# Kernel tuning notes

Measured on AMD Instinct MI355X. Metric: run time of the kernel, lower is better.

The kernel has to match this reference:

```python
import jax, jax.numpy as jnp
import numpy as np
from jax import lax

B, S, H, E, P, K, R = 64, 512, 768, 32, 16, 9, 6
HEADS, C1, C2 = 4, 128, 64
FEAT = 4 * C2 + 1  # e1, e2, e1*e2, context (64 each) + log-distance


def _ln(x, g, b):
    m = x.mean(-1, keepdims=True)
    v = ((x - m) ** 2).mean(-1, keepdims=True)
    return (x - m) * lax.rsqrt(v + 1e-5) * g + b


def _gat(x, adj, W, a_s, a_d, bias, heads, cout, concat):
    # Dense GATConv over a small fully-masked entity graph. adj[b,i,j]=edge j->i (incl. self-loops).
    h = jnp.einsum('bef,fhc->behc', x, W.reshape(x.shape[-1], heads, cout))
    s = jnp.einsum('behc,hc->bhe', h, a_s)  # source-node attention term
    d = jnp.einsum('behc,hc->bhe', h, a_d)  # target-node attention term
    logits = jax.nn.leaky_relu(d[:, :, :, None] + s[:, :, None, :], 0.2)  # [b,h,i,j]
    logits = jnp.where(adj[:, None, :, :], logits, -1e9)
    att = jax.nn.softmax(logits, axis=-1)
    out = jnp.einsum('bhij,bjhc->bihc', att, h)
    out = out.reshape(out.shape[0], out.shape[1], heads * cout) if concat else out.mean(2)
    return out + bias


def _crf_nll(em, tags, mask, start, end, trans):
    # torchcrf: loss = -mean log-likelihood. em [B,S,K]; tags [B,S]; mask [B,S] bool.
    emt = jnp.transpose(em, (1, 0, 2))
    tgt = tags.T
    mkt = mask.T.astype(em.dtype)
    num0 = start[tgt[0]] + jnp.take_along_axis(emt[0], tgt[0][:, None], 1)[:, 0]

    def nstep(c, inp):
        ptag, sc = c
        e, t, m = inp
        step = trans[ptag, t] + jnp.take_along_axis(e, t[:, None], 1)[:, 0]
        return (jnp.where(m > 0, t, ptag), sc + step * m), None

    (ltag, num), _ = lax.scan(nstep, (tgt[0], num0), (emt[1:], tgt[1:], mkt[1:]))
    num = num + end[ltag]
    a0 = start[None, :] + emt[0]

    def dstep(a, inp):
        e, m = inp
        nxt = jax.scipy.special.logsumexp(a[:, :, None] + trans[None] + e[:, None, :], axis=1)
        return jnp.where(m[:, None] > 0, nxt, a), None

    aT, _ = lax.scan(dstep, a0, (emt[1:], mkt[1:]))
    Z = jax.scipy.special.logsumexp(aT + end[None], axis=1)
    return jnp.mean(Z - num)


def setup_inputs() -> dict:
    key = jax.random.key(0)
    ks = jax.random.split(key, 24)
    n = lambda i, shape, s=0.05: jax.random.normal(ks[i], shape, jnp.float32) * s
    return {
        'sequence_output': jax.random.normal(ks[0], (B, S, H), jnp.float32),
        'attention_mask': jnp.ones((B, S), jnp.int32),
        'ner_labels': jax.random.randint(ks[1], (B, S), 0, K),
        'entity_start': jax.random.randint(ks[2], (B, E), 0, S - 8),
        'entity_len': jax.random.randint(ks[3], (B, E), 0, 8),
        'pair_e1': jax.random.randint(ks[4], (B, P), 0, E),
        'pair_e2': jax.random.randint(ks[5], (B, P), 0, E),
        'pair_labels': jax.random.randint(ks[6], (B, P), 0, 2),
        'adj_mask': jnp.ones((B, E, E), bool),
        'w_ner1': n(7, (H, 256)), 'b_ner1': jnp.zeros((256,), jnp.float32),
        'w_ner2': n(8, (256, K)), 'b_ner2': jnp.zeros((K,), jnp.float32),
        'crf_start': n(9, (K,), 0.1), 'crf_end': n(10, (K,), 0.1), 'crf_trans': n(11, (K, K), 0.1),
        'w_gat1': n(12, (H, HEADS * C1)), 'a_src1': n(13, (HEADS, C1)), 'a_dst1': n(14, (HEADS, C1)),
        'b_gat1': jnp.zeros((HEADS * C1,), jnp.float32),
        'w_gat2': n(15, (HEADS * C1, C2)), 'a_src2': n(16, (1, C2)), 'a_dst2': n(17, (1, C2)),
        'b_gat2': jnp.zeros((C2,), jnp.float32),
        'w_fe': n(18, (FEAT, 512)), 'b_fe': jnp.zeros((512,), jnp.float32),
        'g_fe': jnp.ones((512,), jnp.float32), 'be_fe': jnp.zeros((512,), jnp.float32),
        'w_rc1': n(19, (R, 512, 256)), 'b_rc1': jnp.zeros((R, 256), jnp.float32),
        'g_rc': jnp.ones((R, 256), jnp.float32), 'be_rc': jnp.zeros((R, 256), jnp.float32),
        'w_rc2': n(20, (R, 256, 1)), 'b_rc2': jnp.zeros((R,), jnp.float32),
    }


def reference(sequence_output, attention_mask, ner_labels, entity_start, entity_len,
              pair_e1, pair_e2, pair_labels, adj_mask,
              w_ner1, b_ner1, w_ner2, b_ner2, crf_start, crf_end, crf_trans,
              w_gat1, a_src1, a_dst1, b_gat1, w_gat2, a_src2, a_dst2, b_gat2,
              w_fe, b_fe, g_fe, be_fe, w_rc1, b_rc1, g_rc, be_rc, w_rc2, b_rc2):
    # NER head (dropout off / eval)
    ner_logits = jnp.maximum(sequence_output @ w_ner1 + b_ner1, 0.0) @ w_ner2 + b_ner2
    ner_loss = _crf_nll(ner_logits, ner_labels, attention_mask.astype(bool),
                        crf_start, crf_end, crf_trans)
    # entity span mean-pool via inclusive cumsum trick
    cs = jnp.concatenate([jnp.zeros((B, 1, H), sequence_output.dtype),
                          jnp.cumsum(sequence_output, axis=1)], axis=1)
    e_end = jnp.clip(entity_start + entity_len, 0, S - 1)
    seg = (jnp.take_along_axis(cs, (e_end + 1)[:, :, None], 1)
           - jnp.take_along_axis(cs, entity_start[:, :, None], 1))
    ent = seg / (e_end - entity_start + 1).astype(sequence_output.dtype)[:, :, None]  # [B,E,H]
    x = _gat(ent, adj_mask, w_gat1, a_src1, a_dst1, b_gat1, HEADS, C1, True)
    x = jnp.maximum(x, 0.0)
    x = _gat(x, adj_mask, w_gat2, a_src2, a_dst2, b_gat2, 1, C2, False)  # [B,E,64]
    x1 = jnp.take_along_axis(x, pair_e1[:, :, None], 1)
    x2 = jnp.take_along_axis(x, pair_e2[:, :, None], 1)
    ctx = jnp.broadcast_to(x.mean(1, keepdims=True), (B, P, C2))
    dist = jnp.log(jnp.abs(pair_e1 - pair_e2).astype(x.dtype) + 1.0)[:, :, None]
    pf = jnp.concatenate([x1, x2, x1 * x2, ctx, dist], axis=-1)  # [B,P,257]
    fe = jax.nn.leaky_relu(_ln(pf @ w_fe + b_fe, g_fe, be_fe), 0.01)
    h1 = jnp.einsum('bpf,rfo->rbpo', fe, w_rc1) + b_rc1[:, None, None, :]
    h1 = jax.nn.leaky_relu(_ln(h1, g_rc[:, None, None, :], be_rc[:, None, None, :]), 0.01)
    z = jnp.einsum('rbpo,ro->rbp', h1, w_rc2[:, :, 0]) + b_rc2[:, None, None]
    y = pair_labels.astype(z.dtype)[None]
    # BCEWithLogitsLoss(pos_weight=2.0), mean per relation type, summed over types
    bce = -(2.0 * y * jax.nn.log_sigmoid(z) + (1.0 - y) * jax.nn.log_sigmoid(-z))
    rel_loss = bce.mean(axis=(1, 2)).sum()
    total = ner_loss + rel_loss
    return ner_logits, z, total
```

## Files before the change

### kernel.cpp

```cpp
#include <hip/hip_runtime.h>
#include <math.h>


#define NB 64
#define NS 512
#define NH 768
#define NE 32
#define NP 16
#define NK 9
#define NR 6
#define NHEADS 4
#define NC1 128
#define NC2 64
#define SEGS 16
#define SEGLEN 32

#define ZOFF 294912
#define TOTOFF 301056

#define WS_ENT   0u
#define WS_HG1   1572864u
#define WS_X1    2621440u
#define WS_H2    3670016u
#define WS_X2    3801088u
#define WS_S1    3932160u
#define WS_D1    3940352u
#define WS_S2    3948544u
#define WS_D2    3950592u
#define WS_CTX   3952640u
#define WS_PF    3956736u
#define WS_FE    4222976u
#define WS_CRF   4747264u
#define WS_REL   4747328u
#define WS_W1T   4747392u
#define WS_WRT   0u
#define WS_WFET  393216u
#define WS_SEG   475136u

typedef __attribute__((ext_vector_type(8))) short bf16x8;
typedef __attribute__((ext_vector_type(4))) float f32x4;

__device__ __forceinline__ unsigned short f2bf(float x) {
  union { float f; unsigned u; } v; v.f = x;
  unsigned r = v.u + 0x7FFFu + ((v.u >> 16) & 1u);
  return (unsigned short)(r >> 16);
}

__device__ __forceinline__ float logsigf(float x) {
  if (x >= 0.f) return -log1pf(__expf(-x));
  return x - log1pf(__expf(x));
}

__global__ __launch_bounds__(256) void k_w1t(const float* __restrict__ w1,
    unsigned short* __restrict__ w1t) {
  const int k = blockIdx.x, t = threadIdx.x;
  w1t[t * NH + k] = f2bf(w1[k * 256 + t]);
}

__global__ __launch_bounds__(256) void k_wrt(const float* __restrict__ w1,
    unsigned short* __restrict__ wrt) {
  __shared__ unsigned short tr[256 * 72];
  const int r = blockIdx.x >> 3, kt = blockIdx.x & 7;
  const int k0 = kt * 64, t = threadIdx.x;
#pragma unroll
  for (int i = 0; i < 16; i++) {
    const int slot = t + 256 * i;
    const int row = slot >> 6, c4 = slot & 63;
    const float4 f = *reinterpret_cast<const float4*>(
        &w1[((size_t)(r * 512) + k0 + row) * 256 + c4 * 4]);
    tr[(c4 * 4 + 0) * 72 + row] = f2bf(f.x);
    tr[(c4 * 4 + 1) * 72 + row] = f2bf(f.y);
    tr[(c4 * 4 + 2) * 72 + row] = f2bf(f.z);
    tr[(c4 * 4 + 3) * 72 + row] = f2bf(f.w);
  }
  __syncthreads();
#pragma unroll
  for (int i = 0; i < 8; i++) {
    const int slot = t + 256 * i;
    const int col = slot >> 3, q = slot & 7;
    *reinterpret_cast<uint4*>(&wrt[((size_t)(r * 256 + col)) * 512 + k0 + q * 8]) =
        *reinterpret_cast<const uint4*>(&tr[col * 72 + q * 8]);
  }
}

__global__ __launch_bounds__(256) void k_wfet(const float* __restrict__ w,
    unsigned short* __restrict__ wt) {
  __shared__ unsigned short tr[256 * 72];
  const int kt = blockIdx.x % 5, cb = blockIdx.x / 5;
  const int k0 = kt * 64, c0 = cb * 256, t = threadIdx.x;
#pragma unroll
  for (int i = 0; i < 16; i++) {
    const int slot = t + 256 * i;
    const int row = slot >> 6, c4 = slot & 63;
    const int k = k0 + row;
    float4 f = {0.f, 0.f, 0.f, 0.f};
    if (k < 257)
      f = *reinterpret_cast<const float4*>(&w[(size_t)k * 512 + c0 + c4 * 4]);
    tr[(c4 * 4 + 0) * 72 + row] = f2bf(f.x);
    tr[(c4 * 4 + 1) * 72 + row] = f2bf(f.y);
    tr[(c4 * 4 + 2) * 72 + row] = f2bf(f.z);
    tr[(c4 * 4 + 3) * 72 + row] = f2bf(f.w);
  }
  __syncthreads();
#pragma unroll
  for (int i = 0; i < 8; i++) {
    const int slot = t + 256 * i;
    const int col = slot >> 3, q = slot & 7;
    *reinterpret_cast<uint4*>(&wt[((size_t)(c0 + col)) * 320 + k0 + q * 8]) =
        *reinterpret_cast<const uint4*>(&tr[col * 72 + q * 8]);
  }
}

__global__ __launch_bounds__(256) void k_ner(const float* __restrict__ seq,
    const unsigned short* __restrict__ w1t, const float* __restrict__ b1,
    const float* __restrict__ w2, const float* __restrict__ b2,
    float* __restrict__ out) {
  __shared__ unsigned short AsS[64 * 40];
  __shared__ unsigned short BsS[256 * 40];
  __shared__ float zs[64 * 4 * 12];
  const int t = threadIdx.x;
  const int tok0 = blockIdx.x * 64;
  const int w = t >> 6, lane = t & 63, quad = lane >> 4, l15 = lane & 15;

  f32x4 acc[4][4];
#pragma unroll
  for (int r = 0; r < 4; r++)
#pragma unroll
    for (int c = 0; c < 4; c++) acc[r][c] = (f32x4){0.f, 0.f, 0.f, 0.f};

  const int tokA = t >> 2, koffA = (t & 3) * 8;
  const float* aptr = seq + (size_t)(tok0 + tokA) * NH + koffA;

  for (int kt = 0; kt < NH; kt += 32) {
    __syncthreads();
    {
      const float4 f0 = *reinterpret_cast<const float4*>(aptr + kt);
      const float4 f1 = *reinterpret_cast<const float4*>(aptr + kt + 4);
      bf16x8 av;
      av[0] = (short)f2bf(f0.x); av[1] = (short)f2bf(f0.y);
      av[2] = (short)f2bf(f0.z); av[3] = (short)f2bf(f0.w);
      av[4] = (short)f2bf(f1.x); av[5] = (short)f2bf(f1.y);
      av[6] = (short)f2bf(f1.z); av[7] = (short)f2bf(f1.w);
      *reinterpret_cast<bf16x8*>(&AsS[tokA * 40 + koffA]) = av;
    }
#pragma unroll
    for (int i = 0; i < 4; i++) {
      const int q = t + 256 * i;
      const int col = q >> 2, koff = (q & 3) * 8;
      *reinterpret_cast<uint4*>(&BsS[col * 40 + koff]) =
          *reinterpret_cast<const uint4*>(&w1t[(size_t)col * NH + kt + koff]);
    }
    __syncthreads();
    bf16x8 a[4], b[4];
#pragma unroll
    for (int r = 0; r < 4; r++)
      a[r] = *reinterpret_cast<const bf16x8*>(&AsS[(r * 16 + l15) * 40 + quad * 8]);
#pragma unroll
    for (int c = 0; c < 4; c++)
      b[c] = *reinterpret_cast<const bf16x8*>(&BsS[(w * 64 + c * 16 + l15) * 40 + quad * 8]);
#pragma unroll
    for (int r = 0; r < 4; r++)
#pragma unroll
      for (int c = 0; c < 4; c++)
        acc[r][c] = __builtin_amdgcn_mfma_f32_16x16x32_bf16(a[r], b[c], acc[r][c], 0, 0, 0);
  }

  float b1v[4], w2v[4][NK];
#pragma unroll
  for (int c = 0; c < 4; c++) {
    const int col = w * 64 + c * 16 + l15;
    b1v[c] = b1[col];
#pragma unroll
    for (int cc = 0; cc < NK; cc++) w2v[c][cc] = w2[col * NK + cc];
  }
#pragma unroll
  for (int r = 0; r < 4; r++) {
#pragma unroll
    for (int reg = 0; reg < 4; reg++) {
      float p[NK];
#pragma unroll
      for (int cc = 0; cc < NK; cc++) p[cc] = 0.f;
#pragma unroll
      for (int c = 0; c < 4; c++) {
        const float h = fmaxf(acc[r][c][reg] + b1v[c], 0.f);
#pragma unroll
        for (int cc = 0; cc < NK; cc++) p[cc] = fmaf(h, w2v[c][cc], p[cc]);
      }
#pragma unroll
      for (int o = 1; o < 16; o <<= 1)
#pragma unroll
        for (int cc = 0; cc < NK; cc++) p[cc] += __shfl_xor(p[cc], o);
      if (l15 == 0) {
        const int tokr = r * 16 + quad * 4 + reg;
#pragma unroll
        for (int cc = 0; cc < NK; cc++) zs[(tokr * 4 + w) * 12 + cc] = p[cc];
      }
    }
  }
  __syncthreads();
  if (t < 64) {
#pragma unroll
    for (int cc = 0; cc < NK; cc++) {
      const float z = zs[(t * 4 + 0) * 12 + cc] + zs[(t * 4 + 1) * 12 + cc] +
                      zs[(t * 4 + 2) * 12 + cc] + zs[(t * 4 + 3) * 12 + cc] + b2[cc];
      out[(size_t)(tok0 + t) * NK + cc] = z;
    }
  }
}

__global__ __launch_bounds__(128) void k_crf_seg(const float* __restrict__ em,
    const int* __restrict__ mask, const float* __restrict__ trans,
    float* __restrict__ segm) {
  __shared__ float bufA[16 * 81];
  __shared__ float bufB[8 * 81];
  __shared__ float ems[SEGLEN * 9];
  __shared__ int mks[SEGLEN];
  __shared__ float trs[81];
  const int blk = blockIdx.x;
  const int b = blk >> 4, seg = blk & 15;
  const int t = threadIdx.x;
  const int s0 = 1 + seg * SEGLEN;
  const float* emb = em + (size_t)b * NS * NK;
  const int* mk = mask + b * NS;
  if (t < 81) trs[t] = trans[t];
  for (int i = t; i < SEGLEN * 9; i += 128) {
    const int g = s0 * 9 + i;
    ems[i] = (g < NS * 9) ? emb[g] : 0.f;
  }
  if (t < SEGLEN) {
    const int s = s0 + t;
    mks[t] = (s < NS) ? mk[s] : 0;
  }
  __syncthreads();
  for (int idx = t; idx < 16 * 81; idx += 128) {
    const int p = idx / 81, e = idx % 81, i = e / 9, j = e % 9;
    const int la = 2 * p, lb = la + 1;
    const bool ma = mks[la] > 0, mb = mks[lb] > 0;
    float r;
    if (ma && mb) {
      float v[9], mx = -1e30f;
#pragma unroll
      for (int m = 0; m < 9; m++) {
        v[m] = trs[i * 9 + m] + ems[la * 9 + m] + trs[m * 9 + j];
        mx = fmaxf(mx, v[m]);
      }
      float sum = 0.f;
#pragma unroll
      for (int m = 0; m < 9; m++) sum += __expf(v[m] - mx);
      r = mx + __logf(sum) + ems[lb * 9 + j];
    } else if (ma) {
      r = trs[e] + ems[la * 9 + j];
    } else if (mb) {
      r = trs[e] + ems[lb * 9 + j];
    } else {
      r = (i == j) ? 0.f : -1e30f;
    }
    bufA[p * 81 + e] = r;
  }
  float* src = bufA;
  float* dst = bufB;
  for (int n = 16; n > 1; n >>= 1) {
    __syncthreads();
    const int half = n >> 1;
    for (int idx = t; idx < half * 81; idx += 128) {
      const int q = idx / 81, e = idx % 81, i = e / 9, j = e % 9;
      const float* A = src + (size_t)(2 * q) * 81;
      const float* Bm = src + (size_t)(2 * q + 1) * 81;
      float v[9], mx = -1e30f;
#pragma unroll
      for (int m = 0; m < 9; m++) {
        v[m] = A[i * 9 + m] + Bm[m * 9 + j];
        mx = fmaxf(mx, v[m]);
      }
      float sum = 0.f;
#pragma unroll
      for (int m = 0; m < 9; m++) sum += __expf(v[m] - mx);
      dst[q * 81 + e] = mx + __logf(sum);
    }
    float* tmp = src; src = dst; dst = tmp;
  }
  __syncthreads();
  if (t < 81) segm[((size_t)b * SEGS + seg) * 81 + t] = src[t];
}

__global__ __launch_bounds__(64) void k_crf_fin(const float* __restrict__ em,
    const int* __restrict__ tags, const int* __restrict__ mask,
    const float* __restrict__ startv, const float* __restrict__ endv,
    const float* __restrict__ trans, const float* __restrict__ segm,
    float* __restrict__ lossb) {
  __shared__ float sm[SEGS * 81];
  __shared__ float av[16];
  __shared__ float red[2];
  const int b = blockIdx.x, t = threadIdx.x;
  const float* emb = em + (size_t)b * NS * NK;
  const int* mk = mask + b * NS;
  const int* tg = tags + b * NS;
  for (int i = t; i < SEGS * 81; i += 64) sm[i] = segm[(size_t)b * SEGS * 81 + i];
  {
    float num = 0.f;
    int lastS = 0;
#pragma unroll
    for (int o = 0; o < 8; o++) {
      const int s = t * 8 + o;
      if (s >= 1 && mk[s] > 0) {
        const int cur = tg[s], prv = tg[s - 1];
        num += trans[prv * NK + cur] + emb[s * NK + cur];
        lastS = s;
      }
    }
#pragma unroll
    for (int o = 32; o > 0; o >>= 1) {
      num += __shfl_xor(num, o);
      lastS = max(lastS, __shfl_xor(lastS, o));
    }
    if (t == 0) {
      const int t0 = tg[0];
      red[0] = startv[t0] + emb[t0] + num + endv[tg[lastS]];
    }
  }
  __syncthreads();
  if (t < 9) av[t] = startv[t] + emb[t];
  __syncthreads();
  for (int h = 0; h < SEGS; h++) {
    float nv = 0.f;
    if (t < 9) {
      float v[9], mx = -1e30f;
#pragma unroll
      for (int i2 = 0; i2 < 9; i2++) {
        v[i2] = av[i2] + sm[h * 81 + i2 * 9 + t];
        mx = fmaxf(mx, v[i2]);
      }
      float sum = 0.f;
#pragma unroll
      for (int i2 = 0; i2 < 9; i2++) sum += __expf(v[i2] - mx);
      nv = mx + __logf(sum);
    }
    __syncthreads();
    if (t < 9) av[t] = nv;
    __syncthreads();
  }
  if (t == 0) {
    float mx = -1e30f;
#pragma unroll
    for (int j = 0; j < 9; j++) mx = fmaxf(mx, av[j] + endv[j]);
    float sum = 0.f;
#pragma unroll
    for (int j = 0; j < 9; j++) sum += __expf(av[j] + endv[j] - mx);
    lossb[b] = (mx + __logf(sum)) - red[0];
  }
}

__global__ __launch_bounds__(256) void k_ent(const float* __restrict__ seq,
    const int* __restrict__ est, const int* __restrict__ elen, float* __restrict__ ent) {
  const int be = blockIdx.x;
  const int b = be >> 5, e = be & 31;
  const int st = est[b * NE + e];
  int en = st + elen[b * NE + e];
  en = min(max(en, 0), NS - 1);
  const float inv = 1.f / (float)(en - st + 1);
  for (int c = threadIdx.x; c < NH; c += 256) {
    float s = 0.f;
    for (int r = st; r <= en; r++) s += seq[((size_t)b * NS + r) * NH + c];
    ent[((size_t)b * NE + e) * NH + c] = s * inv;
  }
}

__global__ __launch_bounds__(256) void k_g1(const float* __restrict__ ent,
    const float* __restrict__ w, float* __restrict__ hout) {
  __shared__ float As[32 * 36];
  __shared__ float Bs[32 * 128];
  const int b = blockIdx.x >> 2, cb = blockIdx.x & 3;
  const int t = threadIdx.x;
  const int tc = t & 31, tr = t >> 5;
  float acc[4][4];
#pragma unroll
  for (int i = 0; i < 4; i++)
#pragma unroll
    for (int j = 0; j < 4; j++) acc[i][j] = 0.f;
  for (int kt = 0; kt < NH; kt += 32) {
    __syncthreads();
    {
      const int e = t >> 3, k4 = t & 7;
      *reinterpret_cast<float4*>(&As[e * 36 + k4 * 4]) =
          *reinterpret_cast<const float4*>(&ent[((size_t)b * NE + e) * NH + kt + k4 * 4]);
    }
#pragma unroll
    for (int i = 0; i < 4; i++) {
      const int slot = t + 256 * i;
      const int row = slot >> 5, cg = slot & 31;
      *reinterpret_cast<float4*>(&Bs[row * 128 + cg * 4]) =
          *reinterpret_cast<const float4*>(&w[(size_t)(kt + row) * 512 + cb * 128 + cg * 4]);
    }
    __syncthreads();
#pragma unroll
    for (int kg = 0; kg < 8; kg++) {
      float4 a[4];
#pragma unroll
      for (int i = 0; i < 4; i++)
        a[i] = *reinterpret_cast<const float4*>(&As[(tr * 4 + i) * 36 + kg * 4]);
#pragma unroll
      for (int k2 = 0; k2 < 4; k2++) {
        const float4 bv = *reinterpret_cast<const float4*>(&Bs[(kg * 4 + k2) * 128 + tc * 4]);
#pragma unroll
        for (int i = 0; i < 4; i++) {
          const float av = reinterpret_cast<const float*>(&a[i])[k2];
          acc[i][0] = fmaf(av, bv.x, acc[i][0]);
          acc[i][1] = fmaf(av, bv.y, acc[i][1]);
          acc[i][2] = fmaf(av, bv.z, acc[i][2]);
          acc[i][3] = fmaf(av, bv.w, acc[i][3]);
        }
      }
    }
  }
#pragma unroll
  for (int i = 0; i < 4; i++) {
    float4 v;
    v.x = acc[i][0]; v.y = acc[i][1]; v.z = acc[i][2]; v.w = acc[i][3];
    *reinterpret_cast<float4*>(&hout[((size_t)b * NE + tr * 4 + i) * 512 + cb * 128 + tc * 4]) = v;
  }
}

__global__ __launch_bounds__(128) void k_sd1(const float* __restrict__ h,
    const float* __restrict__ as, const float* __restrict__ ad,
    float* __restrict__ s1, float* __restrict__ d1) {
  __shared__ float sm[4];
  const int be = blockIdx.x;
  const int b = be >> 5, e = be & 31;
  const int t = threadIdx.x;
  for (int hd = 0; hd < NHEADS; hd++) {
    const float v = h[((size_t)b * NE + e) * 512 + hd * NC1 + t];
    float sv = v * as[hd * NC1 + t];
    float dv = v * ad[hd * NC1 + t];
#pragma unroll
    for (int o = 32; o > 0; o >>= 1) { sv += __shfl_xor(sv, o); dv += __shfl_xor(dv, o); }
    if ((t & 63) == 0) { sm[(t >> 6) * 2] = sv; sm[(t >> 6) * 2 + 1] = dv; }
    __syncthreads();
    if (t == 0) {
      s1[(b * NHEADS + hd) * NE + e] = sm[0] + sm[2];
      d1[(b * NHEADS + hd) * NE + e] = sm[1] + sm[3];
    }
    __syncthreads();
  }
}

__global__ __launch_bounds__(128) void k_att1(const float* __restrict__ h,
    const float* __restrict__ s1, const float* __restrict__ d1,
    const unsigned char* __restrict__ adj, const float* __restrict__ bias,
    float* __restrict__ x1) {
  __shared__ float att[NE];
  const int blk = blockIdx.x;
  const int i = blk & 31, hd = (blk >> 5) & 3, b = blk >> 7;
  const int t = threadIdx.x;
  if (t < NE) {
    float lg = d1[(b * NHEADS + hd) * NE + i] + s1[(b * NHEADS + hd) * NE + t];
    lg = lg >= 0.f ? lg : 0.2f * lg;
    if (!adj[((size_t)b * NE + i) * NE + t]) lg = -1e9f;
    att[t] = lg;
  }
  __syncthreads();
  if (t == 0) {
    float m = -1e30f;
#pragma unroll
    for (int j = 0; j < NE; j++) m = fmaxf(m, att[j]);
    float ex[NE];
    float sum = 0.f;
#pragma unroll
    for (int j = 0; j < NE; j++) { ex[j] = __expf(att[j] - m); sum += ex[j]; }
    const float inv = 1.f / sum;
#pragma unroll
    for (int j = 0; j < NE; j++) att[j] = ex[j] * inv;
  }
  __syncthreads();
  float acc = bias[hd * NC1 + t];
  for (int j = 0; j < NE; j++)
    acc += att[j] * h[((size_t)b * NE + j) * 512 + hd * NC1 + t];
  x1[((size_t)b * NE + i) * 512 + hd * NC1 + t] = fmaxf(acc, 0.f);
}

__global__ __launch_bounds__(256) void k_g2(const float* __restrict__ x1,
    const float* __restrict__ w, const float* __restrict__ as, const float* __restrict__ ad,
    float* __restrict__ h2, float* __restrict__ s2, float* __restrict__ d2) {
  __shared__ float As[32 * 36];
  __shared__ float Bs[32 * 64];
  const int b = blockIdx.x;
  const int t = threadIdx.x;
  const int tc = t & 15, tr = t >> 4;
  float acc[2][4];
#pragma unroll
  for (int i = 0; i < 2; i++)
#pragma unroll
    for (int j = 0; j < 4; j++) acc[i][j] = 0.f;
  for (int kt = 0; kt < 512; kt += 32) {
    __syncthreads();
    {
      const int e = t >> 3, k4 = t & 7;
      *reinterpret_cast<float4*>(&As[e * 36 + k4 * 4]) =
          *reinterpret_cast<const float4*>(&x1[((size_t)b * NE + e) * 512 + kt + k4 * 4]);
    }
#pragma unroll
    for (int i = 0; i < 2; i++) {
      const int slot = t + 256 * i;
      const int row = slot >> 4, cg = slot & 15;
      *reinterpret_cast<float4*>(&Bs[row * 64 + cg * 4]) =
          *reinterpret_cast<const float4*>(&w[(size_t)(kt + row) * NC2 + cg * 4]);
    }
    __syncthreads();
#pragma unroll
    for (int kg = 0; kg < 8; kg++) {
      float4 a[2];
#pragma unroll
      for (int i = 0; i < 2; i++)
        a[i] = *reinterpret_cast<const float4*>(&As[(tr * 2 + i) * 36 + kg * 4]);
#pragma unroll
      for (int k2 = 0; k2 < 4; k2++) {
        const float4 bv = *reinterpret_cast<const float4*>(&Bs[(kg * 4 + k2) * 64 + tc * 4]);
#pragma unroll
        for (int i = 0; i < 2; i++) {
          const float av = reinterpret_cast<const float*>(&a[i])[k2];
          acc[i][0] = fmaf(av, bv.x, acc[i][0]);
          acc[i][1] = fmaf(av, bv.y, acc[i][1]);
          acc[i][2] = fmaf(av, bv.z, acc[i][2]);
          acc[i][3] = fmaf(av, bv.w, acc[i][3]);
        }
      }
    }
  }
  const float4 a4s = *reinterpret_cast<const float4*>(&as[tc * 4]);
  const float4 a4d = *reinterpret_cast<const float4*>(&ad[tc * 4]);
#pragma unroll
  for (int i = 0; i < 2; i++) {
    const int e = tr * 2 + i;
    float4 v;
    v.x = acc[i][0]; v.y = acc[i][1]; v.z = acc[i][2]; v.w = acc[i][3];
    *reinterpret_cast<float4*>(&h2[((size_t)b * NE + e) * NC2 + tc * 4]) = v;
    float sv = v.x * a4s.x + v.y * a4s.y + v.z * a4s.z + v.w * a4s.w;
    float dv = v.x * a4d.x + v.y * a4d.y + v.z * a4d.z + v.w * a4d.w;
#pragma unroll
    for (int o = 8; o > 0; o >>= 1) { sv += __shfl_xor(sv, o); dv += __shfl_xor(dv, o); }
    if (tc == 0) { s2[b * NE + e] = sv; d2[b * NE + e] = dv; }
  }
}

__global__ __launch_bounds__(64) void k_att2(const float* __restrict__ h2,
    const float* __restrict__ s2, const float* __restrict__ d2,
    const unsigned char* __restrict__ adj, const float* __restrict__ bias,
    float* __restrict__ x2) {
  __shared__ float att[NE];
  const int be = blockIdx.x;
  const int b = be >> 5, i = be & 31;
  const int t = threadIdx.x;
  if (t < NE) {
    float lg = d2[b * NE + i] + s2[b * NE + t];
    lg = lg >= 0.f ? lg : 0.2f * lg;
    if (!adj[((size_t)b * NE + i) * NE + t]) lg = -1e9f;
    att[t] = lg;
  }
  __syncthreads();
  if (t == 0) {
    float m = -1e30f;
#pragma unroll
    for (int j = 0; j < NE; j++) m = fmaxf(m, att[j]);
    float ex[NE];
    float sum = 0.f;
#pragma unroll
    for (int j = 0; j < NE; j++) { ex[j] = __expf(att[j] - m); sum += ex[j]; }
    const float inv = 1.f / sum;
#pragma unroll
    for (int j = 0; j < NE; j++) att[j] = ex[j] * inv;
  }
  __syncthreads();
  float acc = bias[t];
  for (int j = 0; j < NE; j++)
    acc += att[j] * h2[((size_t)b * NE + j) * NC2 + t];
  x2[((size_t)b * NE + i) * NC2 + t] = acc;
}

__global__ __launch_bounds__(64) void k_ctx(const float* __restrict__ x2, float* __restrict__ ctx) {
  const int b = blockIdx.x, t = threadIdx.x;
  float s = 0.f;
  for (int e = 0; e < NE; e++) s += x2[((size_t)b * NE + e) * NC2 + t];
  ctx[b * NC2 + t] = s * (1.f / NE);
}

__global__ __launch_bounds__(64) void k_pf(const float* __restrict__ x2,
    const float* __restrict__ ctx, const int* __restrict__ pe1, const int* __restrict__ pe2,
    float* __restrict__ pf) {
  const int bp = blockIdx.x;
  const int b = bp >> 4, p = bp & 15;
  const int t = threadIdx.x;
  const int e1 = pe1[b * NP + p], e2 = pe2[b * NP + p];
  const float v1 = x2[((size_t)b * NE + e1) * NC2 + t];
  const float v2 = x2[((size_t)b * NE + e2) * NC2 + t];
  float* row = pf + (size_t)bp * 260;
  row[t] = v1;
  row[64 + t] = v2;
  row[128 + t] = v1 * v2;
  row[192 + t] = ctx[b * NC2 + t];
  if (t == 0) row[256] = logf(fabsf((float)(e1 - e2)) + 1.f);
  if (t < 3) row[257 + t] = 0.f;
}

__global__ __launch_bounds__(256) void k_fe(const float* __restrict__ pf,
    const unsigned short* __restrict__ wt, const float* __restrict__ bfe,
    const float* __restrict__ g, const float* __restrict__ be,
    unsigned short* __restrict__ feb) {
  __shared__ unsigned short Af[16 * 320];
  __shared__ float Cs[16 * 520];
  const int b = blockIdx.x, t = threadIdx.x;
  const int w = t >> 6, lane = t & 63, quad = lane >> 4, l15 = lane & 15;
  for (int i = t; i < 16 * 320; i += 256) {
    const int p = i / 320, k = i - p * 320;
    Af[i] = (k < 260) ? f2bf(pf[(size_t)(b * NP + p) * 260 + k]) : (unsigned short)0;
  }
  __syncthreads();
  f32x4 acc[8];
#pragma unroll
  for (int c = 0; c < 8; c++) acc[c] = (f32x4){0.f, 0.f, 0.f, 0.f};
#pragma unroll
  for (int kt = 0; kt < 10; kt++) {
    const bf16x8 a = *reinterpret_cast<const bf16x8*>(&Af[l15 * 320 + kt * 32 + quad * 8]);
#pragma unroll
    for (int c = 0; c < 8; c++) {
      const int col = w * 128 + c * 16 + l15;
      const bf16x8 bv = *reinterpret_cast<const bf16x8*>(&wt[(size_t)col * 320 + kt * 32 + quad * 8]);
      acc[c] = __builtin_amdgcn_mfma_f32_16x16x32_bf16(a, bv, acc[c], 0, 0, 0);
    }
  }
#pragma unroll
  for (int c = 0; c < 8; c++)
#pragma unroll
    for (int reg = 0; reg < 4; reg++)
      Cs[(quad * 4 + reg) * 520 + w * 128 + c * 16 + l15] = acc[c][reg];
  __syncthreads();
  float bfev[8], gv[8], bev[8];
#pragma unroll
  for (int ch = 0; ch < 8; ch++) {
    const int col = ch * 64 + lane;
    bfev[ch] = bfe[col]; gv[ch] = g[col]; bev[ch] = be[col];
  }
#pragma unroll
  for (int pp = 0; pp < 4; pp++) {
    const int p = w * 4 + pp;
    float v[8], s = 0.f, sq = 0.f;
#pragma unroll
    for (int ch = 0; ch < 8; ch++) {
      v[ch] = Cs[p * 520 + ch * 64 + lane] + bfev[ch];
      s += v[ch]; sq += v[ch] * v[ch];
    }
#pragma unroll
    for (int o = 32; o > 0; o >>= 1) { s += __shfl_xor(s, o); sq += __shfl_xor(sq, o); }
    const float mean = s * (1.f / 512.f);
    const float var = sq * (1.f / 512.f) - mean * mean;
    const float rr = rsqrtf(var + 1e-5f);
#pragma unroll
    for (int ch = 0; ch < 8; ch++) {
      float n = (v[ch] - mean) * rr * gv[ch] + bev[ch];
      n = n >= 0.f ? n : 0.01f * n;
      feb[(size_t)(b * NP + p) * 512 + ch * 64 + lane] = f2bf(n);
    }
  }
}

__global__ __launch_bounds__(256) void k_rc(const unsigned short* __restrict__ feb,
    const unsigned short* __restrict__ wrt, const float* __restrict__ b1,
    const float* __restrict__ g, const float* __restrict__ be,
    const float* __restrict__ w2, const float* __restrict__ b2,
    const int* __restrict__ ylab, float* __restrict__ zout, float* __restrict__ relacc) {
  __shared__ unsigned short Af[16 * 520];
  __shared__ float Cs[16 * 264];
  const int blk = blockIdx.x;
  const int r = blk >> 6, b = blk & 63;
  const int t = threadIdx.x;
  const int w = t >> 6, lane = t & 63, quad = lane >> 4, l15 = lane & 15;
#pragma unroll
  for (int i = 0; i < 4; i++) {
    const int slot = t + 256 * i;
    const int p = slot >> 6, q = slot & 63;
    *reinterpret_cast<uint4*>(&Af[p * 520 + q * 8]) =
        *reinterpret_cast<const uint4*>(&feb[(size_t)(b * NP + p) * 512 + q * 8]);
  }
  __syncthreads();
  f32x4 acc[4];
#pragma unroll
  for (int c = 0; c < 4; c++) acc[c] = (f32x4){0.f, 0.f, 0.f, 0.f};
#pragma unroll
  for (int kt = 0; kt < 16; kt++) {
    const bf16x8 a = *reinterpret_cast<const bf16x8*>(&Af[l15 * 520 + kt * 32 + quad * 8]);
#pragma unroll
    for (int c = 0; c < 4; c++) {
      const int col = w * 64 + c * 16 + l15;
      const bf16x8 bv = *reinterpret_cast<const bf16x8*>(
          &wrt[(size_t)(r * 256 + col) * 512 + kt * 32 + quad * 8]);
      acc[c] = __builtin_amdgcn_mfma_f32_16x16x32_bf16(a, bv, acc[c], 0, 0, 0);
    }
  }
#pragma unroll
  for (int c = 0; c < 4; c++)
#pragma unroll
    for (int reg = 0; reg < 4; reg++)
      Cs[(quad * 4 + reg) * 264 + w * 64 + c * 16 + l15] = acc[c][reg];
  __syncthreads();
  float b1v[4], gv[4], bev[4], w2v[4];
#pragma unroll
  for (int ch = 0; ch < 4; ch++) {
    const int col = r * 256 + ch * 64 + lane;
    b1v[ch] = b1[col]; gv[ch] = g[col]; bev[ch] = be[col]; w2v[ch] = w2[col];
  }
  const float b2v = b2[r];
  float local = 0.f;
#pragma unroll
  for (int pp = 0; pp < 4; pp++) {
    const int p = w * 4 + pp;
    float v[4], s = 0.f, sq = 0.f;
#pragma unroll
    for (int ch = 0; ch < 4; ch++) {
      v[ch] = Cs[p * 264 + ch * 64 + lane] + b1v[ch];
      s += v[ch]; sq += v[ch] * v[ch];
    }
#pragma unroll
    for (int o = 32; o > 0; o >>= 1) { s += __shfl_xor(s, o); sq += __shfl_xor(sq, o); }
    const float mean = s * (1.f / 256.f);
    const float var = sq * (1.f / 256.f) - mean * mean;
    const float rr = rsqrtf(var + 1e-5f);
    float zdot = 0.f;
#pragma unroll
    for (int ch = 0; ch < 4; ch++) {
      float n = (v[ch] - mean) * rr * gv[ch] + bev[ch];
      n = n >= 0.f ? n : 0.01f * n;
      zdot = fmaf(n, w2v[ch], zdot);
    }
#pragma unroll
    for (int o = 32; o > 0; o >>= 1) zdot += __shfl_xor(zdot, o);
    if (lane == 0) {
      const float zp = zdot + b2v;
      zout[(size_t)(r * NB + b) * NP + p] = zp;
      const float y = (float)ylab[b * NP + p];
      local += -(2.f * y * logsigf(zp) + (1.f - y) * logsigf(-zp));
    }
  }
  if (lane == 0) atomicAdd(relacc, local * (1.f / (NB * NP)));
}

__global__ __launch_bounds__(64) void k_fin(const float* __restrict__ lossb,
    const float* __restrict__ rel, float* __restrict__ out) {
  float v = lossb[threadIdx.x];
#pragma unroll
  for (int o = 32; o > 0; o >>= 1) v += __shfl_down(v, o);
  if (threadIdx.x == 0) out[TOTOFF] = v * (1.f / NB) + rel[0];
}

extern "C" void kernel_launch(void* const* d_in, const int* in_sizes, int n_in,
                              void* d_out, int out_size, void* d_ws, size_t ws_size,
                              hipStream_t stream) {
  const float* seq = (const float*)d_in[0];
  const int* amask = (const int*)d_in[1];
  const int* nlab = (const int*)d_in[2];
  const int* est = (const int*)d_in[3];
  const int* elen = (const int*)d_in[4];
  const int* pe1 = (const int*)d_in[5];
  const int* pe2 = (const int*)d_in[6];
  const int* plab = (const int*)d_in[7];
  const unsigned char* adj = (const unsigned char*)d_in[8];
  const float* w_ner1 = (const float*)d_in[9];
  const float* b_ner1 = (const float*)d_in[10];
  const float* w_ner2 = (const float*)d_in[11];
  const float* b_ner2 = (const float*)d_in[12];
  const float* crf_start = (const float*)d_in[13];
  const float* crf_end = (const float*)d_in[14];
  const float* crf_trans = (const float*)d_in[15];
  const float* w_gat1 = (const float*)d_in[16];
  const float* a_src1 = (const float*)d_in[17];
  const float* a_dst1 = (const float*)d_in[18];
  const float* b_gat1 = (const float*)d_in[19];
  const float* w_gat2 = (const float*)d_in[20];
  const float* a_src2 = (const float*)d_in[21];
  const float* a_dst2 = (const float*)d_in[22];
  const float* b_gat2 = (const float*)d_in[23];
  const float* w_fe = (const float*)d_in[24];
  const float* b_fe = (const float*)d_in[25];
  const float* g_fe = (const float*)d_in[26];
  const float* be_fe = (const float*)d_in[27];
  const float* w_rc1 = (const float*)d_in[28];
  const float* b_rc1 = (const float*)d_in[29];
  const float* g_rc = (const float*)d_in[30];
  const float* be_rc = (const float*)d_in[31];
  const float* w_rc2 = (const float*)d_in[32];
  const float* b_rc2 = (const float*)d_in[33];

  float* out = (float*)d_out;
  float* ws = (float*)d_ws;
  float* ent = ws + WS_ENT;
  float* hg1 = ws + WS_HG1;
  float* x1 = ws + WS_X1;
  float* h2 = ws + WS_H2;
  float* x2 = ws + WS_X2;
  float* s1 = ws + WS_S1;
  float* d1 = ws + WS_D1;
  float* s2 = ws + WS_S2;
  float* d2 = ws + WS_D2;
  float* ctx = ws + WS_CTX;
  float* pf = ws + WS_PF;
  float* crfb = ws + WS_CRF;
  float* rel = ws + WS_REL;
  unsigned short* w1t = (unsigned short*)(ws + WS_W1T);
  unsigned short* feb = (unsigned short*)(ws + WS_FE);
  unsigned short* wrt = (unsigned short*)(ws + WS_WRT);
  unsigned short* wfet = (unsigned short*)(ws + WS_WFET);
  float* segm = ws + WS_SEG;

  hipMemsetAsync(rel, 0, sizeof(float), stream);

  k_w1t<<<NH, 256, 0, stream>>>(w_ner1, w1t);
  k_ner<<<512, 256, 0, stream>>>(seq, w1t, b_ner1, w_ner2, b_ner2, out);
  k_ent<<<NB * NE, 256, 0, stream>>>(seq, est, elen, ent);
  k_g1<<<NB * 4, 256, 0, stream>>>(ent, w_gat1, hg1);
  k_wrt<<<NR * 8, 256, 0, stream>>>(w_rc1, wrt);
  k_wfet<<<10, 256, 0, stream>>>(w_fe, wfet);
  k_crf_seg<<<NB * SEGS, 128, 0, stream>>>(out, amask, crf_trans, segm);
  k_crf_fin<<<NB, 64, 0, stream>>>(out, nlab, amask, crf_start, crf_end, crf_trans,
                                   segm, crfb);
  k_sd1<<<NB * NE, 128, 0, stream>>>(hg1, a_src1, a_dst1, s1, d1);
  k_att1<<<NB * NHEADS * NE, 128, 0, stream>>>(hg1, s1, d1, adj, b_gat1, x1);
  k_g2<<<NB, 256, 0, stream>>>(x1, w_gat2, a_src2, a_dst2, h2, s2, d2);
  k_att2<<<NB * NE, 64, 0, stream>>>(h2, s2, d2, adj, b_gat2, x2);
  k_ctx<<<NB, 64, 0, stream>>>(x2, ctx);
  k_pf<<<NB * NP, 64, 0, stream>>>(x2, ctx, pe1, pe2, pf);
  k_fe<<<NB, 256, 0, stream>>>(pf, wfet, b_fe, g_fe, be_fe, feb);
  k_rc<<<NR * NB, 256, 0, stream>>>(feb, wrt, b_rc1, g_rc, be_rc, w_rc2, b_rc2,
                                    plab, out + ZOFF, rel);
  k_fin<<<1, 64, 0, stream>>>(crfb, rel, out);
}
```

Measured before the change: 444.1 us.

## Double-buffer NER GEMM A tile and load B fragments directly from global

Reworks the NER projection GEMM main loop. The activation tile now goes into shared memory as fp32 in a double buffer with an XOR swizzle, and is converted to bf16 when read. Weight fragments are loaded straight from global into registers and prefetched one k-step ahead, so the B tile no longer passes through shared memory. This leaves one barrier per iteration and overlaps global loads with MFMA work, at the cost of more registers and redundant bf16 conversion across waves.

Measured after the change: 450.0 us. No clear change (+1.3%).

```diff
diff --git a/kernel.cpp b/kernel.cpp
--- a/kernel.cpp
+++ b/kernel.cpp
@@ -115,54 +115,87 @@
     const unsigned short* __restrict__ w1t, const float* __restrict__ b1,
     const float* __restrict__ w2, const float* __restrict__ b2,
     float* __restrict__ out) {
-  __shared__ unsigned short AsS[64 * 40];
-  __shared__ unsigned short BsS[256 * 40];
+  __shared__ float As[2][64 * 32];
   __shared__ float zs[64 * 4 * 12];
   const int t = threadIdx.x;
   const int tok0 = blockIdx.x * 64;
   const int w = t >> 6, lane = t & 63, quad = lane >> 4, l15 = lane & 15;
 
+  const int srow = t >> 2, ssg = t & 3;
+  const float* gA = seq + (size_t)(tok0 + srow) * NH + ssg * 8;
+  const int wslot = (2 * ssg) ^ (srow & 7);
+  const int wofs0 = srow * 32 + wslot * 4;
+  const int wofs1 = srow * 32 + (wslot ^ 1) * 4;
+
+  int rofs[4][2];
+#pragma unroll
+  for (int r = 0; r < 4; r++) {
+    const int row = r * 16 + l15;
+    const int s0 = (2 * quad) ^ (l15 & 7);
+    rofs[r][0] = row * 32 + s0 * 4;
+    rofs[r][1] = row * 32 + (s0 ^ 1) * 4;
+  }
+
+  const unsigned short* gB[4];
+#pragma unroll
+  for (int c = 0; c < 4; c++)
+    gB[c] = w1t + (size_t)(w * 64 + c * 16 + l15) * NH + quad * 8;
+
   f32x4 acc[4][4];
 #pragma unroll
   for (int r = 0; r < 4; r++)
 #pragma unroll
     for (int c = 0; c < 4; c++) acc[r][c] = (f32x4){0.f, 0.f, 0.f, 0.f};
 
-  const int tokA = t >> 2, koffA = (t & 3) * 8;
-  const float* aptr = seq + (size_t)(tok0 + tokA) * NH + koffA;
-
-  for (int kt = 0; kt < NH; kt += 32) {
-    __syncthreads();
-    {
-      const float4 f0 = *reinterpret_cast<const float4*>(aptr + kt);
-      const float4 f1 = *reinterpret_cast<const float4*>(aptr + kt + 4);
+  bf16x8 bcur[4];
+  {
+    const float4 a0 = *reinterpret_cast<const float4*>(gA);
+    const float4 a1 = *reinterpret_cast<const float4*>(gA + 4);
+#pragma unroll
+    for (int c = 0; c < 4; c++)
+      bcur[c] = *reinterpret_cast<const bf16x8*>(gB[c]);
+    *reinterpret_cast<float4*>(&As[0][wofs0]) = a0;
+    *reinterpret_cast<float4*>(&As[0][wofs1]) = a1;
+  }
+  __syncthreads();
+
+  for (int kt = 0; kt < 24; kt++) {
+    const int cur = kt & 1;
+    float* Ac = &As[cur][0];
+    float* An = &As[cur ^ 1][0];
+    float4 na0, na1;
+    bf16x8 bnext[4];
+    if (kt < 23) {
+      na0 = *reinterpret_cast<const float4*>(gA + (kt + 1) * 32);
+      na1 = *reinterpret_cast<const float4*>(gA + (kt + 1) * 32 + 4);
+#pragma unroll
+      for (int c = 0; c < 4; c++)
+        bnext[c] = *reinterpret_cast<const bf16x8*>(gB[c] + (kt + 1) * 32);
+    }
+    bf16x8 a[4];
+#pragma unroll
+    for (int r = 0; r < 4; r++) {
+      const float4 f0 = *reinterpret_cast<const float4*>(&Ac[rofs[r][0]]);
+      const float4 f1 = *reinterpret_cast<const float4*>(&Ac[rofs[r][1]]);
       bf16x8 av;
       av[0] = (short)f2bf(f0.x); av[1] = (short)f2bf(f0.y);
       av[2] = (short)f2bf(f0.z); av[3] = (short)f2bf(f0.w);
       av[4] = (short)f2bf(f1.x); av[5] = (short)f2bf(f1.y);
       av[6] = (short)f2bf(f1.z); av[7] = (short)f2bf(f1.w);
-      *reinterpret_cast<bf16x8*>(&AsS[tokA * 40 + koffA]) = av;
-    }
-#pragma unroll
-    for (int i = 0; i < 4; i++) {
-      const int q = t + 256 * i;
-      const int col = q >> 2, koff = (q & 3) * 8;
-      *reinterpret_cast<uint4*>(&BsS[col * 40 + koff]) =
-          *reinterpret_cast<const uint4*>(&w1t[(size_t)col * NH + kt + koff]);
-    }
-    __syncthreads();
-    bf16x8 a[4], b[4];
+      a[r] = av;
+    }
 #pragma unroll
     for (int r = 0; r < 4; r++)
-      a[r] = *reinterpret_cast<const bf16x8*>(&AsS[(r * 16 + l15) * 40 + quad * 8]);
-#pragma unroll
-    for (int c = 0; c < 4; c++)
-      b[c] = *reinterpret_cast<const bf16x8*>(&BsS[(w * 64 + c * 16 + l15) * 40 + quad * 8]);
-#pragma unroll
-    for (int r = 0; r < 4; r++)
 #pragma unroll
       for (int c = 0; c < 4; c++)
-        acc[r][c] = __builtin_amdgcn_mfma_f32_16x16x32_bf16(a[r], b[c], acc[r][c], 0, 0, 0);
+        acc[r][c] = __builtin_amdgcn_mfma_f32_16x16x32_bf16(a[r], bcur[c], acc[r][c], 0, 0, 0);
+    if (kt < 23) {
+      *reinterpret_cast<float4*>(&An[wofs0]) = na0;
+      *reinterpret_cast<float4*>(&An[wofs1]) = na1;
+#pragma unroll
+      for (int c = 0; c < 4; c++) bcur[c] = bnext[c];
+    }
+    __syncthreads();
   }
 
   float b1v[4], w2v[4][NK];
```

## Pipeline NER GEMM with register prefetch and direct-from-global B fragments

Applied to the files above, without the earlier changes.

Rewrites the NER projection GEMM so each block handles 32 tokens instead of 64, doubling the grid. The weight (B) fragments are loaded straight from global memory into registers with a three-stage prefetch, removing the shared-memory staging of B. The activation tile is double-buffered in LDS with loads prefetched three steps ahead, leaving one barrier per k-step instead of two. The trade-off is more redundant global reads of the weights across blocks, since each block now re-reads all of w1t for fewer tokens, plus higher register pressure.

Measured after the change: 464.6 us. 4.6% more time.

```diff
diff --git a/kernel.cpp b/kernel.cpp
--- a/kernel.cpp
+++ b/kernel.cpp
@@ -115,54 +115,72 @@
     const unsigned short* __restrict__ w1t, const float* __restrict__ b1,
     const float* __restrict__ w2, const float* __restrict__ b2,
     float* __restrict__ out) {
-  __shared__ unsigned short AsS[64 * 40];
-  __shared__ unsigned short BsS[256 * 40];
-  __shared__ float zs[64 * 4 * 12];
+  __shared__ unsigned short As[2][32 * 40];
+  __shared__ float zs[32 * 4 * 12];
   const int t = threadIdx.x;
-  const int tok0 = blockIdx.x * 64;
+  const int tok0 = blockIdx.x * 32;
   const int w = t >> 6, lane = t & 63, quad = lane >> 4, l15 = lane & 15;
 
-  f32x4 acc[4][4];
-#pragma unroll
-  for (int r = 0; r < 4; r++)
+  const int srow = t >> 3, sk4 = t & 7;
+  const float* gA = seq + (size_t)(tok0 + srow) * NH + sk4 * 4;
+  const int wofs = srow * 40 + sk4 * 4;
+
+  const unsigned short* gB[4];
+#pragma unroll
+  for (int c = 0; c < 4; c++)
+    gB[c] = w1t + (size_t)(w * 64 + c * 16 + l15) * NH + quad * 8;
+
+  f32x4 acc[2][4];
+#pragma unroll
+  for (int r = 0; r < 2; r++)
 #pragma unroll
     for (int c = 0; c < 4; c++) acc[r][c] = (f32x4){0.f, 0.f, 0.f, 0.f};
 
-  const int tokA = t >> 2, koffA = (t & 3) * 8;
-  const float* aptr = seq + (size_t)(tok0 + tokA) * NH + koffA;
-
-  for (int kt = 0; kt < NH; kt += 32) {
-    __syncthreads();
-    {
-      const float4 f0 = *reinterpret_cast<const float4*>(aptr + kt);
-      const float4 f1 = *reinterpret_cast<const float4*>(aptr + kt + 4);
-      bf16x8 av;
-      av[0] = (short)f2bf(f0.x); av[1] = (short)f2bf(f0.y);
-      av[2] = (short)f2bf(f0.z); av[3] = (short)f2bf(f0.w);
-      av[4] = (short)f2bf(f1.x); av[5] = (short)f2bf(f1.y);
-      av[6] = (short)f2bf(f1.z); av[7] = (short)f2bf(f1.w);
-      *reinterpret_cast<bf16x8*>(&AsS[tokA * 40 + koffA]) = av;
-    }
-#pragma unroll
-    for (int i = 0; i < 4; i++) {
-      const int q = t + 256 * i;
-      const int col = q >> 2, koff = (q & 3) * 8;
-      *reinterpret_cast<uint4*>(&BsS[col * 40 + koff]) =
-          *reinterpret_cast<const uint4*>(&w1t[(size_t)col * NH + kt + koff]);
-    }
-    __syncthreads();
-    bf16x8 a[4], b[4];
-#pragma unroll
-    for (int r = 0; r < 4; r++)
-      a[r] = *reinterpret_cast<const bf16x8*>(&AsS[(r * 16 + l15) * 40 + quad * 8]);
-#pragma unroll
-    for (int c = 0; c < 4; c++)
-      b[c] = *reinterpret_cast<const bf16x8*>(&BsS[(w * 64 + c * 16 + l15) * 40 + quad * 8]);
-#pragma unroll
-    for (int r = 0; r < 4; r++)
+  float4 ast[4];
+  bf16x8 bb[3][4];
+
+  ast[0] = *reinterpret_cast<const float4*>(gA);
+  ast[1] = *reinterpret_cast<const float4*>(gA + 32);
+  ast[2] = *reinterpret_cast<const float4*>(gA + 64);
+#pragma unroll
+  for (int c = 0; c < 4; c++) bb[0][c] = *reinterpret_cast<const bf16x8*>(gB[c]);
+#pragma unroll
+  for (int c = 0; c < 4; c++) bb[1][c] = *reinterpret_cast<const bf16x8*>(gB[c] + 32);
+  {
+    const float4 f = ast[0];
+    uint2 v;
+    v.x = (unsigned)f2bf(f.x) | ((unsigned)f2bf(f.y) << 16);
+    v.y = (unsigned)f2bf(f.z) | ((unsigned)f2bf(f.w) << 16);
+    *reinterpret_cast<uint2*>(&As[0][wofs]) = v;
+  }
+  asm volatile("s_waitcnt lgkmcnt(0)" ::: "memory");
+  __builtin_amdgcn_s_barrier();
+
+#pragma unroll
+  for (int kt = 0; kt < 24; kt++) {
+    if (kt < 21)
+      ast[(kt + 3) & 3] = *reinterpret_cast<const float4*>(gA + (kt + 3) * 32);
+    if (kt < 22) {
 #pragma unroll
       for (int c = 0; c < 4; c++)
-        acc[r][c] = __builtin_amdgcn_mfma_f32_16x16x32_bf16(a[r], b[c], acc[r][c], 0, 0, 0);
+        bb[(kt + 2) % 3][c] = *reinterpret_cast<const bf16x8*>(gB[c] + (kt + 2) * 32);
+    }
+    const bf16x8 a0 = *reinterpret_cast<const bf16x8*>(&As[kt & 1][l15 * 40 + quad * 8]);
+    const bf16x8 a1 = *reinterpret_cast<const bf16x8*>(&As[kt & 1][(16 + l15) * 40 + quad * 8]);
+#pragma unroll
+    for (int c = 0; c < 4; c++) {
+      acc[0][c] = __builtin_amdgcn_mfma_f32_16x16x32_bf16(a0, bb[kt % 3][c], acc[0][c], 0, 0, 0);
+      acc[1][c] = __builtin_amdgcn_mfma_f32_16x16x32_bf16(a1, bb[kt % 3][c], acc[1][c], 0, 0, 0);
+    }
+    if (kt < 23) {
+      const float4 f = ast[(kt + 1) & 3];
+      uint2 v;
+      v.x = (unsigned)f2bf(f.x) | ((unsigned)f2bf(f.y) << 16);
+      v.y = (unsigned)f2bf(f.z) | ((unsigned)f2bf(f.w) << 16);
+      *reinterpret_cast<uint2*>(&As[(kt + 1) & 1][wofs]) = v;
+    }
+    asm volatile("s_waitcnt lgkmcnt(0)" ::: "memory");
+    __builtin_amdgcn_s_barrier();
   }
 
   float b1v[4], w2v[4][NK];
@@ -174,7 +192,7 @@
     for (int cc = 0; cc < NK; cc++) w2v[c][cc] = w2[col * NK + cc];
   }
 #pragma unroll
-  for (int r = 0; r < 4; r++) {
+  for (int r = 0; r < 2; r++) {
 #pragma unroll
     for (int reg = 0; reg < 4; reg++) {
       float p[NK];
@@ -198,7 +216,7 @@
     }
   }
   __syncthreads();
-  if (t < 64) {
+  if (t < 32) {
 #pragma unroll
     for (int cc = 0; cc < NK; cc++) {
       const float z = zs[(t * 4 + 0) * 12 + cc] + zs[(t * 4 + 1) * 12 + cc] +
@@ -811,7 +829,7 @@
   hipMemsetAsync(rel, 0, sizeof(float), stream);
 
   k_w1t<<<NH, 256, 0, stream>>>(w_ner1, w1t);
-  k_ner<<<512, 256, 0, stream>>>(seq, w1t, b_ner1, w_ner2, b_ner2, out);
+  k_ner<<<1024, 256, 0, stream>>>(seq, w1t, b_ner1, w_ner2, b_ner2, out);
   k_ent<<<NB * NE, 256, 0, stream>>>(seq, est, elen, ent);
   k_g1<<<NB * 4, 256, 0, stream>>>(ent, w_gat1, hg1);
   k_wrt<<<NR * 8, 256, 0, stream>>>(w_rc1, wrt);
```

## Rewrite NER GEMM as single-wave LDS-free kernel with pre-swizzled bf16 weights

Applied to the files above, without the earlier changes.

The NER projection GEMM now runs as one 64-thread wave per 32 tokens covering all 256 output columns. MFMA fragments are loaded straight from global memory: activations are converted with packed v_cvt_pk_bf16_f32, and the weights are pre-laid-out by a new swizzle kernel so each lane's fragment is contiguous. This removes the shared-memory staging, the barriers and the cross-wave LDS reduction of the classifier head. In exchange it uses many more registers (a 32-entry accumulator array) and reads weights from L2 again in every block, with no software pipelining of the global loads.

Measured after the change: 523.7 us. 1.18x slower.

```diff
diff --git a/kernel.cpp b/kernel.cpp
--- a/kernel.cpp
+++ b/kernel.cpp
@@ -46,15 +46,33 @@
   return (unsigned short)(r >> 16);
 }
 
+__device__ __forceinline__ unsigned cvt2bf(float lo, float hi) {
+  unsigned r;
+  asm("v_cvt_pk_bf16_f32 %0, %1, %2" : "=v"(r) : "v"(lo), "v"(hi));
+  return r;
+}
+
+__device__ __forceinline__ bf16x8 packbf8(float4 f0, float4 f1) {
+  union { unsigned u[4]; bf16x8 v; } r;
+  r.u[0] = cvt2bf(f0.x, f0.y);
+  r.u[1] = cvt2bf(f0.z, f0.w);
+  r.u[2] = cvt2bf(f1.x, f1.y);
+  r.u[3] = cvt2bf(f1.z, f1.w);
+  return r.v;
+}
+
 __device__ __forceinline__ float logsigf(float x) {
   if (x >= 0.f) return -log1pf(__expf(-x));
   return x - log1pf(__expf(x));
 }
 
-__global__ __launch_bounds__(256) void k_w1t(const float* __restrict__ w1,
-    unsigned short* __restrict__ w1t) {
-  const int k = blockIdx.x, t = threadIdx.x;
-  w1t[t * NH + k] = f2bf(w1[k * 256 + t]);
+__global__ __launch_bounds__(256) void k_w1s(const float* __restrict__ w1,
+    unsigned short* __restrict__ w1s) {
+  const int b = blockIdx.x, t = threadIdx.x;
+  union { unsigned short s[8]; uint4 u; } v;
+#pragma unroll
+  for (int j = 0; j < 8; j++) v.s[j] = f2bf(w1[(size_t)(b * 8 + j) * 256 + t]);
+  *reinterpret_cast<uint4*>(&w1s[((size_t)(b * 256) + t) * 8]) = v.u;
 }
 
 __global__ __launch_bounds__(256) void k_wrt(const float* __restrict__ w1,
@@ -111,100 +129,88 @@
   }
 }
 
-__global__ __launch_bounds__(256) void k_ner(const float* __restrict__ seq,
-    const unsigned short* __restrict__ w1t, const float* __restrict__ b1,
+__global__ __launch_bounds__(64, 2) void k_ner(const float* __restrict__ seq,
+    const unsigned short* __restrict__ w1s, const float* __restrict__ b1,
     const float* __restrict__ w2, const float* __restrict__ b2,
     float* __restrict__ out) {
-  __shared__ unsigned short AsS[64 * 40];
-  __shared__ unsigned short BsS[256 * 40];
-  __shared__ float zs[64 * 4 * 12];
-  const int t = threadIdx.x;
-  const int tok0 = blockIdx.x * 64;
-  const int w = t >> 6, lane = t & 63, quad = lane >> 4, l15 = lane & 15;
-
-  f32x4 acc[4][4];
-#pragma unroll
-  for (int r = 0; r < 4; r++)
-#pragma unroll
-    for (int c = 0; c < 4; c++) acc[r][c] = (f32x4){0.f, 0.f, 0.f, 0.f};
-
-  const int tokA = t >> 2, koffA = (t & 3) * 8;
-  const float* aptr = seq + (size_t)(tok0 + tokA) * NH + koffA;
-
-  for (int kt = 0; kt < NH; kt += 32) {
-    __syncthreads();
-    {
-      const float4 f0 = *reinterpret_cast<const float4*>(aptr + kt);
-      const float4 f1 = *reinterpret_cast<const float4*>(aptr + kt + 4);
-      bf16x8 av;
-      av[0] = (short)f2bf(f0.x); av[1] = (short)f2bf(f0.y);
-      av[2] = (short)f2bf(f0.z); av[3] = (short)f2bf(f0.w);
-      av[4] = (short)f2bf(f1.x); av[5] = (short)f2bf(f1.y);
-      av[6] = (short)f2bf(f1.z); av[7] = (short)f2bf(f1.w);
-      *reinterpret_cast<bf16x8*>(&AsS[tokA * 40 + koffA]) = av;
-    }
-#pragma unroll
-    for (int i = 0; i < 4; i++) {
-      const int q = t + 256 * i;
-      const int col = q >> 2, koff = (q & 3) * 8;
-      *reinterpret_cast<uint4*>(&BsS[col * 40 + koff]) =
-          *reinterpret_cast<const uint4*>(&w1t[(size_t)col * NH + kt + koff]);
-    }
-    __syncthreads();
-    bf16x8 a[4], b[4];
-#pragma unroll
-    for (int r = 0; r < 4; r++)
-      a[r] = *reinterpret_cast<const bf16x8*>(&AsS[(r * 16 + l15) * 40 + quad * 8]);
-#pragma unroll
-    for (int c = 0; c < 4; c++)
-      b[c] = *reinterpret_cast<const bf16x8*>(&BsS[(w * 64 + c * 16 + l15) * 40 + quad * 8]);
-#pragma unroll
-    for (int r = 0; r < 4; r++)
-#pragma unroll
-      for (int c = 0; c < 4; c++)
-        acc[r][c] = __builtin_amdgcn_mfma_f32_16x16x32_bf16(a[r], b[c], acc[r][c], 0, 0, 0);
-  }
-
-  float b1v[4], w2v[4][NK];
-#pragma unroll
-  for (int c = 0; c < 4; c++) {
-    const int col = w * 64 + c * 16 + l15;
-    b1v[c] = b1[col];
-#pragma unroll
-    for (int cc = 0; cc < NK; cc++) w2v[c][cc] = w2[col * NK + cc];
-  }
-#pragma unroll
-  for (int r = 0; r < 4; r++) {
-#pragma unroll
-    for (int reg = 0; reg < 4; reg++) {
-      float p[NK];
-#pragma unroll
-      for (int cc = 0; cc < NK; cc++) p[cc] = 0.f;
-#pragma unroll
-      for (int c = 0; c < 4; c++) {
-        const float h = fmaxf(acc[r][c][reg] + b1v[c], 0.f);
-#pragma unroll
-        for (int cc = 0; cc < NK; cc++) p[cc] = fmaf(h, w2v[c][cc], p[cc]);
+  const int lane = threadIdx.x;
+  const int quad = lane >> 4, l15 = lane & 15;
+  const int tok0 = blockIdx.x * 32;
+
+  const float* gA0 = seq + (size_t)(tok0 + l15) * NH + quad * 8;
+  const float* gA1 = gA0 + (size_t)16 * NH;
+  const unsigned short* gB = w1s + (quad * 256 + l15) * 8;
+
+  f32x4 acc[2][16];
+#pragma unroll
+  for (int r = 0; r < 2; r++)
+#pragma unroll
+    for (int c = 0; c < 16; c++) acc[r][c] = (f32x4){0.f, 0.f, 0.f, 0.f};
+
+#pragma unroll
+  for (int kt = 0; kt < 24; kt++) {
+    const float4 a00 = *reinterpret_cast<const float4*>(gA0 + kt * 32);
+    const float4 a01 = *reinterpret_cast<const float4*>(gA0 + kt * 32 + 4);
+    const float4 a10 = *reinterpret_cast<const float4*>(gA1 + kt * 32);
+    const float4 a11 = *reinterpret_cast<const float4*>(gA1 + kt * 32 + 4);
+    bf16x8 bfr[16];
+#pragma unroll
+    for (int c = 0; c < 16; c++)
+      bfr[c] = *reinterpret_cast<const bf16x8*>(gB + (size_t)kt * 8192 + c * 128);
+    const bf16x8 a0 = packbf8(a00, a01);
+    const bf16x8 a1 = packbf8(a10, a11);
+#pragma unroll
+    for (int c = 0; c < 16; c++) {
+      acc[0][c] = __builtin_amdgcn_mfma_f32_16x16x32_bf16(a0, bfr[c], acc[0][c], 0, 0, 0);
+      acc[1][c] = __builtin_amdgcn_mfma_f32_16x16x32_bf16(a1, bfr[c], acc[1][c], 0, 0, 0);
+    }
+  }
+
+  float p[2][4][NK];
+#pragma unroll
+  for (int r = 0; r < 2; r++)
+#pragma unroll
+    for (int reg = 0; reg < 4; reg++)
+#pragma unroll
+      for (int cc = 0; cc < NK; cc++) p[r][reg][cc] = 0.f;
+
+#pragma unroll
+  for (int c = 0; c < 16; c++) {
+    const int col = c * 16 + l15;
+    const float b1v = b1[col];
+    float w2v[NK];
+#pragma unroll
+    for (int cc = 0; cc < NK; cc++) w2v[cc] = w2[col * NK + cc];
+#pragma unroll
+    for (int r = 0; r < 2; r++)
+#pragma unroll
+      for (int reg = 0; reg < 4; reg++) {
+        const float h = fmaxf(acc[r][c][reg] + b1v, 0.f);
+#pragma unroll
+        for (int cc = 0; cc < NK; cc++) p[r][reg][cc] = fmaf(h, w2v[cc], p[r][reg][cc]);
       }
-#pragma unroll
-      for (int o = 1; o < 16; o <<= 1)
-#pragma unroll
-        for (int cc = 0; cc < NK; cc++) p[cc] += __shfl_xor(p[cc], o);
-      if (l15 == 0) {
-        const int tokr = r * 16 + quad * 4 + reg;
-#pragma unroll
-        for (int cc = 0; cc < NK; cc++) zs[(tokr * 4 + w) * 12 + cc] = p[cc];
+  }
+#pragma unroll
+  for (int o = 1; o < 16; o <<= 1)
+#pragma unroll
+    for (int r = 0; r < 2; r++)
+#pragma unroll
+      for (int reg = 0; reg < 4; reg++)
+#pragma unroll
+        for (int cc = 0; cc < NK; cc++) p[r][reg][cc] += __shfl_xor(p[r][reg][cc], o);
+  if (l15 == 0) {
+    float b2v[NK];
+#pragma unroll
+    for (int cc = 0; cc < NK; cc++) b2v[cc] = b2[cc];
+#pragma unroll
+    for (int r = 0; r < 2; r++)
+#pragma unroll
+      for (int reg = 0; reg < 4; reg++) {
+        const int tok = tok0 + r * 16 + quad * 4 + reg;
+#pragma unroll
+        for (int cc = 0; cc < NK; cc++)
+          out[(size_t)tok * NK + cc] = p[r][reg][cc] + b2v[cc];
       }
-    }
-  }
-  __syncthreads();
-  if (t < 64) {
-#pragma unroll
-    for (int cc = 0; cc < NK; cc++) {
-      const float z = zs[(t * 4 + 0) * 12 + cc] + zs[(t * 4 + 1) * 12 + cc] +
-                      zs[(t * 4 + 2) * 12 + cc] + zs[(t * 4 + 3) * 12 + cc] + b2[cc];
-      out[(size_t)(tok0 + t) * NK + cc] = z;
-    }
   }
 }
 
@@ -802,7 +808,7 @@
   float* pf = ws + WS_PF;
   float* crfb = ws + WS_CRF;
   float* rel = ws + WS_REL;
-  unsigned short* w1t = (unsigned short*)(ws + WS_W1T);
+  unsigned short* w1s = (unsigned short*)(ws + WS_W1T);
   unsigned short* feb = (unsigned short*)(ws + WS_FE);
   unsigned short* wrt = (unsigned short*)(ws + WS_WRT);
   unsigned short* wfet = (unsigned short*)(ws + WS_WFET);
@@ -810,8 +816,8 @@
 
   hipMemsetAsync(rel, 0, sizeof(float), stream);
 
-  k_w1t<<<NH, 256, 0, stream>>>(w_ner1, w1t);
-  k_ner<<<512, 256, 0, stream>>>(seq, w1t, b_ner1, w_ner2, b_ner2, out);
+  k_w1s<<<96, 256, 0, stream>>>(w_ner1, w1s);
+  k_ner<<<1024, 64, 0, stream>>>(seq, w1s, b_ner1, w_ner2, b_ner2, out);
   k_ent<<<NB * NE, 256, 0, stream>>>(seq, est, elen, ent);
   k_g1<<<NB * 4, 256, 0, stream>>>(ent, w_gat1, hg1);
   k_wrt<<<NR * 8, 256, 0, stream>>>(w_rc1, wrt);
```
